# Optimization experiments

Hardware: AMD Instinct MI355X
Metric: run time of the kernel (lower is better)

## Reference

```python
import jax, jax.numpy as jnp
import numpy as np

N = 100_000      # nodes
E = 1_600_000    # edges (avg degree 16)
IN = 128         # in_feats
HID = 256        # hidden_feats
OUT = 160        # final fc output
EPS = 1e-5       # BatchNorm1d eps


def setup_inputs() -> dict:
    key = jax.random.key(0)
    ks = jax.random.split(key, 11)
    s = 0.02
    return {
        "features": jax.random.normal(ks[0], (N, IN), jnp.float32),
        "src": jax.random.randint(ks[1], (E,), 0, N, dtype=jnp.int32),
        "dst": jax.random.randint(ks[2], (E,), 0, N, dtype=jnp.int32),
        "edge_w": jax.random.uniform(ks[3], (E,), jnp.float32),
        "W_self": jax.random.normal(ks[4], (IN, HID), jnp.float32) * s,
        "W_neigh": jax.random.normal(ks[5], (IN, HID), jnp.float32) * s,
        "bias": jnp.zeros((HID,), jnp.float32),
        "gamma": jnp.ones((HID,), jnp.float32),
        "beta": jnp.zeros((HID,), jnp.float32),
        "fc_W": jax.random.normal(ks[6], (HID, OUT), jnp.float32) * s,
        "fc_b": jnp.zeros((OUT,), jnp.float32),
    }


def reference(features, src, dst, edge_w, W_self, W_neigh, bias, gamma, beta, fc_W, fc_b):
    # SAGEConv 'mean' with edge_weight: mean over incoming edges of src_feat * w
    msg = features[src] * edge_w[:, None]                       # [E, IN]
    ssum = jax.ops.segment_sum(msg, dst, num_segments=N)        # [N, IN]
    deg = jax.ops.segment_sum(jnp.ones((E,), features.dtype), dst, num_segments=N)
    neigh = ssum / jnp.maximum(deg, 1.0)[:, None]               # isolated nodes -> 0
    # rst = fc_self(h) + fc_neigh(neigh) + bias, then activation, then norm (DGL order)
    rst = features @ W_self + neigh @ W_neigh + bias            # [N, HID]
    rst = jax.nn.relu(rst)
    mu = rst.mean(axis=0)
    var = rst.var(axis=0)                                       # biased, as BatchNorm1d training
    rst = (rst - mu) * jax.lax.rsqrt(var + EPS) * gamma + beta
    return rst @ fc_W + fc_b                                    # [N, OUT]
```

## Files before the change

### kernel.cpp

```cpp
#include <hip/hip_runtime.h>
#include <hip/hip_fp16.h>

#define N_NODES 100000
#define N_EDGES 1600000
#define IN_F    128
#define HID_F   256
#define OUT_F   160
#define BN_EPS  1e-5f

#define EPB     4096
#define NCHUNK  ((N_EDGES + EPB - 1) / EPB)
#define NBKT    256
#define NPP2    391
#define BCAP2   8192
#define NSUB    (N_NODES / 32)
#define G1_GRID 512
#define NT2     ((N_NODES + 63) / 64)
#define G2_GRID 512
#define CVT_BLOCKS ((N_NODES * IN_F / 8 + 255) / 256)

typedef __attribute__((ext_vector_type(8))) short bf16x8;
typedef __attribute__((ext_vector_type(4))) float f32x4;
typedef __attribute__((ext_vector_type(2))) float f32x2;

static __device__ inline unsigned short f2bf(float x) {
  unsigned u = __float_as_uint(x);
  return (unsigned short)((u + 0x7fffu + ((u >> 16) & 1u)) >> 16);
}
static __device__ inline unsigned f2bf_pair(float lo, float hi) {
  return (unsigned)f2bf(lo) | ((unsigned)f2bf(hi) << 16);
}
static __device__ inline float bf_lo(unsigned u) {
  return __uint_as_float(u << 16);
}
static __device__ inline float bf_hi(unsigned u) {
  return __uint_as_float(u & 0xffff0000u);
}

#if __has_builtin(__builtin_amdgcn_cvt_f32_fp8)
#define FP8_DEC(d, s) __builtin_amdgcn_cvt_f32_fp8((int)(d), (s))
#else
static __device__ inline float FP8_DEC(unsigned d, int s) {
  unsigned b = (d >> (s * 8)) & 0xffu;
  unsigned em = b & 0x7fu;
  float mag = (em >= 8) ? __uint_as_float((em << 20) + (120u << 23))
                        : (float)em * 0.001953125f;
  return (b & 0x80u) ? -mag : mag;
}
#endif

#if __has_builtin(__builtin_amdgcn_cvt_pk_f32_fp8)
template <bool HI>
static __device__ inline f32x2 FP8_DEC2(unsigned d) {
  return __builtin_amdgcn_cvt_pk_f32_fp8((int)d, HI);
}
#else
template <bool HI>
static __device__ inline f32x2 FP8_DEC2(unsigned d) {
  f32x2 r;
  r.x = FP8_DEC(d, HI ? 2 : 0);
  r.y = FP8_DEC(d, HI ? 3 : 1);
  return r;
}
#endif

static __device__ inline void PK_FMA(f32x2& acc, f32x2 a, f32x2 b) {
#if defined(__gfx950__) || defined(__gfx942__) || defined(__gfx90a__) || \
    defined(__gfx940__) || defined(__gfx941__)
  asm("v_pk_fma_f32 %0, %1, %2, %0" : "+v"(acc) : "v"(a), "v"(b));
#else
  acc.x = fmaf(a.x, b.x, acc.x);
  acc.y = fmaf(a.y, b.y, acc.y);
#endif
}

#if __has_builtin(__builtin_amdgcn_cvt_pk_fp8_f32)
static __device__ inline unsigned fp8_pack4(float a, float b, float c, float d) {
  int p = __builtin_amdgcn_cvt_pk_fp8_f32(a, b, 0, false);
  p = __builtin_amdgcn_cvt_pk_fp8_f32(c, d, p, true);
  return (unsigned)p;
}
#else
static __device__ inline unsigned fp8_enc1(float x) {
  unsigned u = __float_as_uint(x);
  unsigned s = (u >> 24) & 0x80u;
  float ax = fabsf(x);
  if (ax >= 448.f) return s | 0x7eu;
  if (ax < 0.015625f) {
    unsigned m = (unsigned)(ax * 512.f + 0.5f);
    return s | (m > 7u ? 7u : m);
  }
  unsigned b = __float_as_uint(ax);
  b += 0x7ffffu + ((b >> 20) & 1u);
  unsigned exp = (b >> 23) - 120u;
  unsigned man = (b >> 20) & 7u;
  return s | (exp << 3) | man;
}
static __device__ inline unsigned fp8_pack4(float a, float b, float c, float d) {
  return fp8_enc1(a) | (fp8_enc1(b) << 8) | (fp8_enc1(c) << 16) |
         (fp8_enc1(d) << 24);
}
#endif

__global__ __launch_bounds__(256) void k_bucket(
    const int* __restrict__ src, const int* __restrict__ dst,
    const float* __restrict__ ew, int* __restrict__ gcnt,
    uint2* __restrict__ bucket) {
  __shared__ int bcnt[NBKT];
  __shared__ int bcur[NBKT];
  const int tid = threadIdx.x;
  const int e0 = blockIdx.x * EPB;
  bcnt[tid] = 0;
  __syncthreads();
  int ed[16];
  unsigned pd[16];
#pragma unroll
  for (int i = 0; i < 16; ++i) {
    int e = e0 + i * 256 + tid;
    int d = -1;
    unsigned p = 0;
    if (e < N_EDGES) {
      d = dst[e];
      unsigned hb = (unsigned)__half_as_ushort(__float2half(ew[e])) & 0x7fffu;
      p = ((unsigned)src[e] << 15) | hb;
      atomicAdd(&bcnt[d / NPP2], 1);
    }
    ed[i] = d;
    pd[i] = p;
  }
  __syncthreads();
  bcur[tid] = atomicAdd(&gcnt[tid], bcnt[tid]);
  __syncthreads();
#pragma unroll
  for (int i = 0; i < 16; ++i) {
    if (ed[i] >= 0) {
      int b = ed[i] / NPP2;
      int pos = atomicAdd(&bcur[b], 1);
      if (pos < BCAP2)
        bucket[(size_t)b * BCAP2 + pos] = make_uint2((unsigned)ed[i], pd[i]);
    }
  }
}

__global__ __launch_bounds__(256) void k_csr(
    const uint2* __restrict__ bucket, const int* __restrict__ gcnt,
    int* __restrict__ offs, unsigned* __restrict__ pairs) {
  __shared__ int cnt[512];
  __shared__ int wred[4];
  const int b = blockIdx.x;
  const int tid = threadIdx.x;
  const int lo = b * NPP2;
  const int n = min(gcnt[b], BCAP2);
  const uint2* bp = bucket + (size_t)b * BCAP2;

  int v = (tid < b) ? gcnt[tid] : 0;
  int x = v;
#pragma unroll
  for (int off = 1; off < 64; off <<= 1) x += __shfl_xor(x, off, 64);
  if ((tid & 63) == 0) wred[tid >> 6] = x;
  cnt[tid] = 0;
  cnt[tid + 256] = 0;
  __syncthreads();
  const int base = wred[0] + wred[1] + wred[2] + wred[3];

  for (int i = tid; i < n; i += 256)
    atomicAdd(&cnt[(int)bp[i].x - lo], 1);
  __syncthreads();

  if (tid < 64) {
    int carry = 0;
#pragma unroll
    for (int c = 0; c < 8; ++c) {
      int cv = cnt[c * 64 + tid];
      int cx = cv;
#pragma unroll
      for (int off = 1; off < 64; off <<= 1) {
        int q = __shfl_up(cx, off, 64);
        if (tid >= off) cx += q;
      }
      cnt[c * 64 + tid] = carry + cx - cv;
      carry += __shfl(cx, 63, 64);
    }
  }
  __syncthreads();

  for (int j = tid; j < NPP2; j += 256) {
    int node = lo + j;
    if (node < N_NODES) offs[node] = base + cnt[j];
  }
  if (b == 0 && tid == 0) offs[N_NODES] = N_EDGES;
  __syncthreads();

  for (int i = tid; i < n; i += 256) {
    uint2 it = bp[i];
    int r = atomicAdd(&cnt[(int)it.x - lo], 1);
    pairs[base + r] = it.y;
  }
}

__global__ __launch_bounds__(256) void k_convert(
    const float* __restrict__ feat, unsigned* __restrict__ A1u,
    unsigned* __restrict__ Af8u, const float* __restrict__ Wself,
    const float* __restrict__ Wneigh, unsigned short* __restrict__ W1T) {
  if (blockIdx.x >= CVT_BLOCKS) {
    int c = blockIdx.x - CVT_BLOCKS;
    int k = threadIdx.x;
    float v = (k < 128) ? Wself[(size_t)k * HID_F + c]
                        : Wneigh[(size_t)(k - 128) * HID_F + c];
    W1T[(size_t)c * 256 + k] = f2bf(v);
    return;
  }
  long long idx = (long long)blockIdx.x * 256 + threadIdx.x;
  long long fidx = idx * 8;
  if (fidx >= (long long)N_NODES * IN_F) return;
  int node = (int)(fidx >> 7);
  int c0 = (int)(fidx & 127);
  float4 f0 = *reinterpret_cast<const float4*>(feat + fidx);
  float4 f1 = *reinterpret_cast<const float4*>(feat + fidx + 4);
  uint4 o;
  o.x = f2bf_pair(f0.x, f0.y);
  o.y = f2bf_pair(f0.z, f0.w);
  o.z = f2bf_pair(f1.x, f1.y);
  o.w = f2bf_pair(f1.z, f1.w);
  *reinterpret_cast<uint4*>(A1u + (size_t)node * 128 + (c0 >> 1)) = o;
  uint2 q;
  q.x = fp8_pack4(f0.x, f0.y, f0.z, f0.w);
  q.y = fp8_pack4(f1.x, f1.y, f1.z, f1.w);
  *reinterpret_cast<uint2*>(Af8u + (size_t)node * 32 + (c0 >> 2)) = q;
}

__global__ __launch_bounds__(256) void k_gather(
    const int* __restrict__ offs, const unsigned* __restrict__ pairs,
    const unsigned* __restrict__ Af8u, unsigned* __restrict__ A1u) {
  int node = blockIdx.x * 4 + (threadIdx.x >> 6);
  if (node >= N_NODES) return;
  const int lane = threadIdx.x & 63;
  const int g = lane >> 4;
  const int cl = lane & 15;
  const int start = offs[node], end = offs[node + 1];
  const int deg = end - start;
  const unsigned* fbase = Af8u + cl * 2;

  f32x2 acc2[4];
#pragma unroll
  for (int i = 0; i < 4; ++i) acc2[i] = (f32x2){0.f, 0.f};

  for (int k0 = start; k0 < end; k0 += 64) {
    unsigned pr = 0;
    if (k0 + lane < end) pr = pairs[k0 + lane];
    const int cnt = min(64, end - k0);
    const int nsteps = (cnt + 3) >> 2;
    for (int t = 0; t < nsteps; t += 2) {
      unsigned uu0 = (unsigned)__shfl((int)pr, 4 * t + g, 64);
      unsigned uu1 = (unsigned)__shfl((int)pr, 4 * (t + 1) + g, 64);
      int s0 = (int)(uu0 >> 15);
      int s1 = (int)(uu1 >> 15);
      float w0 = __half2float(__ushort_as_half((unsigned short)(uu0 & 0x7fffu)));
      float w1 = __half2float(__ushort_as_half((unsigned short)(uu1 & 0x7fffu)));
      f32x2 wv0 = (f32x2){w0, w0};
      f32x2 wv1 = (f32x2){w1, w1};
      uint2 f0 = *reinterpret_cast<const uint2*>(fbase + (size_t)s0 * 32);
      uint2 f1 = *reinterpret_cast<const uint2*>(fbase + (size_t)s1 * 32);
      PK_FMA(acc2[0], wv0, FP8_DEC2<false>(f0.x));
      PK_FMA(acc2[1], wv0, FP8_DEC2<true>(f0.x));
      PK_FMA(acc2[2], wv0, FP8_DEC2<false>(f0.y));
      PK_FMA(acc2[3], wv0, FP8_DEC2<true>(f0.y));
      PK_FMA(acc2[0], wv1, FP8_DEC2<false>(f1.x));
      PK_FMA(acc2[1], wv1, FP8_DEC2<true>(f1.x));
      PK_FMA(acc2[2], wv1, FP8_DEC2<false>(f1.y));
      PK_FMA(acc2[3], wv1, FP8_DEC2<true>(f1.y));
    }
  }

#pragma unroll
  for (int i = 0; i < 4; ++i) {
    acc2[i].x += __shfl_xor(acc2[i].x, 16, 64);
    acc2[i].x += __shfl_xor(acc2[i].x, 32, 64);
    acc2[i].y += __shfl_xor(acc2[i].y, 16, 64);
    acc2[i].y += __shfl_xor(acc2[i].y, 32, 64);
  }

  if (g == 0) {
    const float inv = (deg > 0) ? (1.0f / (float)deg) : 0.f;
    uint4 o;
    o.x = f2bf_pair(acc2[0].x * inv, acc2[0].y * inv);
    o.y = f2bf_pair(acc2[1].x * inv, acc2[1].y * inv);
    o.z = f2bf_pair(acc2[2].x * inv, acc2[2].y * inv);
    o.w = f2bf_pair(acc2[3].x * inv, acc2[3].y * inv);
    *reinterpret_cast<uint4*>(A1u + (size_t)node * 128 + 64 + cl * 4) = o;
  }
}

__global__ __launch_bounds__(256, 2) void k_gemm1(
    const unsigned short* __restrict__ A1, const unsigned short* __restrict__ W1T,
    const float* __restrict__ bias, unsigned short* __restrict__ y,
    float* __restrict__ colpart) {
  __shared__ unsigned short sh[4 * 32 * 72];
  const int lane = threadIdx.x & 63;
  const int wid = threadIdx.x >> 6;
  const int l16 = lane & 15, lk = lane >> 4;
  const int h0 = wid * 64;
  unsigned short* shw = sh + wid * 32 * 72;

  bf16x8 wreg[8][4];
#pragma unroll
  for (int ks = 0; ks < 8; ++ks)
#pragma unroll
    for (int m = 0; m < 4; ++m)
      wreg[ks][m] = *reinterpret_cast<const bf16x8*>(
          W1T + (size_t)(h0 + m * 16 + l16) * 256 + ks * 32 + lk * 8);

  float4 bias4[4];
#pragma unroll
  for (int m = 0; m < 4; ++m)
    bias4[m] = *reinterpret_cast<const float4*>(bias + h0 + m * 16 + lk * 4);

  float sacc[4][4] = {};
  float qacc[4][4] = {};

  for (int t = blockIdx.x; t < NSUB; t += G1_GRID) {
    const int nbase = t * 32;
    const unsigned short* arow0 = A1 + (size_t)(nbase + l16) * 256 + lk * 8;
    const unsigned short* arow1 = A1 + (size_t)(nbase + 16 + l16) * 256 + lk * 8;

    f32x4 acc[4][2];
#pragma unroll
    for (int m = 0; m < 4; ++m)
#pragma unroll
      for (int n = 0; n < 2; ++n) acc[m][n] = (f32x4){0.f, 0.f, 0.f, 0.f};

#pragma unroll
    for (int ks = 0; ks < 8; ++ks) {
      bf16x8 a0 = *reinterpret_cast<const bf16x8*>(arow0 + ks * 32);
      bf16x8 a1 = *reinterpret_cast<const bf16x8*>(arow1 + ks * 32);
#pragma unroll
      for (int m = 0; m < 4; ++m) {
        acc[m][0] = __builtin_amdgcn_mfma_f32_16x16x32_bf16(
            wreg[ks][m], a0, acc[m][0], 0, 0, 0);
        acc[m][1] = __builtin_amdgcn_mfma_f32_16x16x32_bf16(
            wreg[ks][m], a1, acc[m][1], 0, 0, 0);
      }
    }

#pragma unroll
    for (int m = 0; m < 4; ++m) {
#pragma unroll
      for (int n = 0; n < 2; ++n) {
        float t0 = fmaxf(acc[m][n][0] + bias4[m].x, 0.f);
        float t1 = fmaxf(acc[m][n][1] + bias4[m].y, 0.f);
        float t2 = fmaxf(acc[m][n][2] + bias4[m].z, 0.f);
        float t3 = fmaxf(acc[m][n][3] + bias4[m].w, 0.f);
        uint2 pk;
        pk.x = f2bf_pair(t0, t1);
        pk.y = f2bf_pair(t2, t3);
        *reinterpret_cast<uint2*>(
            &shw[(n * 16 + l16) * 72 + m * 16 + lk * 4]) = pk;
        sacc[m][0] += t0; sacc[m][1] += t1; sacc[m][2] += t2; sacc[m][3] += t3;
        qacc[m][0] = fmaf(t0, t0, qacc[m][0]);
        qacc[m][1] = fmaf(t1, t1, qacc[m][1]);
        qacc[m][2] = fmaf(t2, t2, qacc[m][2]);
        qacc[m][3] = fmaf(t3, t3, qacc[m][3]);
      }
    }

#pragma unroll
    for (int j = 0; j < 4; ++j) {
      int row = j * 8 + (lane >> 3);
      int chunk = lane & 7;
      uint4 v = *reinterpret_cast<const uint4*>(&shw[row * 72 + chunk * 8]);
      *reinterpret_cast<uint4*>(
          y + (size_t)(nbase + row) * 256 + h0 + chunk * 8) = v;
    }
  }

#pragma unroll
  for (int m = 0; m < 4; ++m) {
#pragma unroll
    for (int r = 0; r < 4; ++r) {
      float s = sacc[m][r], q = qacc[m][r];
      s += __shfl_xor(s, 1, 64); s += __shfl_xor(s, 2, 64);
      s += __shfl_xor(s, 4, 64); s += __shfl_xor(s, 8, 64);
      q += __shfl_xor(q, 1, 64); q += __shfl_xor(q, 2, 64);
      q += __shfl_xor(q, 4, 64); q += __shfl_xor(q, 8, 64);
      if (l16 == 0) {
        int h = h0 + m * 16 + lk * 4 + r;
        colpart[(size_t)blockIdx.x * 512 + h] = s;
        colpart[(size_t)blockIdx.x * 512 + 256 + h] = q;
      }
    }
  }
}

__global__ __launch_bounds__(256) void k_redstats(
    const float* __restrict__ colpart, float* __restrict__ colsum,
    float* __restrict__ colsq) {
  const int h = threadIdx.x;
  float s = 0.f, q = 0.f;
  for (int j = blockIdx.x; j < G1_GRID; j += gridDim.x) {
    s += colpart[(size_t)j * 512 + h];
    q += colpart[(size_t)j * 512 + 256 + h];
  }
  atomicAdd(&colsum[h], s);
  atomicAdd(&colsq[h], q);
}

__global__ __launch_bounds__(256) void k_finalize(
    const float* __restrict__ colsum, const float* __restrict__ colsq,
    const float* __restrict__ gamma, const float* __restrict__ beta,
    const float* __restrict__ fcW, const float* __restrict__ fcb,
    unsigned short* __restrict__ W2T, float* __restrict__ b2) {
  const float invN = 1.0f / (float)N_NODES;
  if (blockIdx.x < 192) {
    int o = blockIdx.x, h = threadIdx.x;
    unsigned short v = 0;
    if (o < OUT_F) {
      float mu = colsum[h] * invN;
      float var = colsq[h] * invN - mu * mu;
      float rs = rsqrtf(var + BN_EPS) * gamma[h];
      v = f2bf(fcW[(size_t)h * OUT_F + o] * rs);
    }
    W2T[(size_t)o * 256 + h] = v;
  } else if (threadIdx.x < OUT_F) {
    int o = threadIdx.x;
    float acc = fcb[o];
    for (int h = 0; h < HID_F; ++h) {
      float mu = colsum[h] * invN;
      float var = colsq[h] * invN - mu * mu;
      float rs = rsqrtf(var + BN_EPS) * gamma[h];
      acc += (beta[h] - mu * rs) * fcW[(size_t)h * OUT_F + o];
    }
    b2[o] = acc;
  }
}

__global__ __launch_bounds__(256, 2) void k_gemm2(
    const unsigned short* __restrict__ y, const unsigned short* __restrict__ W2T,
    const float* __restrict__ b2, float* __restrict__ out) {
  const int lane = threadIdx.x & 63;
  const int wid = threadIdx.x >> 6;
  const int l16 = lane & 15, lk = lane >> 4;
  const int wn = wid & 1;
  const int o0 = (wid >> 1) * 80;

  bf16x8 wreg[8][5];
#pragma unroll
  for (int ks = 0; ks < 8; ++ks)
#pragma unroll
    for (int m = 0; m < 5; ++m)
      wreg[ks][m] = *reinterpret_cast<const bf16x8*>(
          W2T + (size_t)(o0 + m * 16 + l16) * 256 + ks * 32 + lk * 8);

  float4 b24[5];
#pragma unroll
  for (int m = 0; m < 5; ++m)
    b24[m] = *reinterpret_cast<const float4*>(b2 + o0 + m * 16 + lk * 4);

  for (int t = blockIdx.x; t < NT2; t += G2_GRID) {
    const int nb = t * 64 + wn * 32;
    const int r0 = min(nb + l16, N_NODES - 1);
    const int r1 = min(nb + 16 + l16, N_NODES - 1);

    f32x4 acc[5][2];
#pragma unroll
    for (int m = 0; m < 5; ++m)
#pragma unroll
      for (int n = 0; n < 2; ++n) acc[m][n] = (f32x4){0.f, 0.f, 0.f, 0.f};

#pragma unroll
    for (int ks = 0; ks < 8; ++ks) {
      bf16x8 bf0 = *reinterpret_cast<const bf16x8*>(
          y + (size_t)r0 * 256 + ks * 32 + lk * 8);
      bf16x8 bf1 = *reinterpret_cast<const bf16x8*>(
          y + (size_t)r1 * 256 + ks * 32 + lk * 8);
#pragma unroll
      for (int m = 0; m < 5; ++m) {
        acc[m][0] = __builtin_amdgcn_mfma_f32_16x16x32_bf16(
            wreg[ks][m], bf0, acc[m][0], 0, 0, 0);
        acc[m][1] = __builtin_amdgcn_mfma_f32_16x16x32_bf16(
            wreg[ks][m], bf1, acc[m][1], 0, 0, 0);
      }
    }

#pragma unroll
    for (int n = 0; n < 2; ++n) {
      const int fb = nb + n * 16;
      if (fb < N_NODES) {
#pragma unroll
        for (int m = 0; m < 5; ++m) {
          float4 v;
          v.x = acc[m][n][0] + b24[m].x;
          v.y = acc[m][n][1] + b24[m].y;
          v.z = acc[m][n][2] + b24[m].z;
          v.w = acc[m][n][3] + b24[m].w;
          *reinterpret_cast<float4*>(
              out + (size_t)(fb + l16) * OUT_F + o0 + m * 16 + lk * 4) = v;
        }
      }
    }
  }
}

extern "C" void kernel_launch(void* const* d_in, const int* in_sizes, int n_in,
                              void* d_out, int out_size, void* d_ws,
                              size_t ws_size, hipStream_t stream) {
  const float* feat   = (const float*)d_in[0];
  const int*   src    = (const int*)d_in[1];
  const int*   dst    = (const int*)d_in[2];
  const float* ew     = (const float*)d_in[3];
  const float* Wself  = (const float*)d_in[4];
  const float* Wneigh = (const float*)d_in[5];
  const float* bias   = (const float*)d_in[6];
  const float* gamma  = (const float*)d_in[7];
  const float* beta   = (const float*)d_in[8];
  const float* fcW    = (const float*)d_in[9];
  const float* fcb    = (const float*)d_in[10];
  float* out = (float*)d_out;

  char* ws = (char*)d_ws;
  int*            gcnt    = (int*)(ws + 0);
  float*          colsum  = (float*)(ws + 1024);
  float*          colsq   = (float*)(ws + 2048);
  int*            offs    = (int*)(ws + 4224);
  unsigned*       pairs   = (unsigned*)(ws + 404480);
  uint2*          bucket  = (uint2*)(ws + 6804480);
  unsigned*       Af8u    = (unsigned*)(ws + 23581696);
  unsigned*       A1u     = (unsigned*)(ws + 36381696);
  unsigned short* A1      = (unsigned short*)(ws + 36381696);
  unsigned short* W1T     = (unsigned short*)(ws + 87581696);
  unsigned short* W2T     = (unsigned short*)(ws + 87712768);
  float*          b2      = (float*)(ws + 87811072);
  unsigned short* y       = (unsigned short*)(ws + 87811712);
  float*          colpart = (float*)(ws + 139011712);

  hipMemsetAsync(ws, 0, 3072, stream);

  dim3 b256(256);
  k_convert<<<dim3(CVT_BLOCKS + 256), b256, 0, stream>>>(
      feat, A1u, Af8u, Wself, Wneigh, W1T);
  k_bucket<<<dim3(NCHUNK), b256, 0, stream>>>(src, dst, ew, gcnt, bucket);
  k_csr<<<dim3(NBKT), b256, 0, stream>>>(bucket, gcnt, offs, pairs);
  k_gather<<<dim3((N_NODES + 3) / 4), b256, 0, stream>>>(
      offs, pairs, Af8u, A1u);
  k_gemm1<<<dim3(G1_GRID), b256, 0, stream>>>(A1, W1T, bias, y, colpart);
  k_redstats<<<dim3(32), b256, 0, stream>>>(colpart, colsum, colsq);
  k_finalize<<<dim3(193), b256, 0, stream>>>(
      colsum, colsq, gamma, beta, fcW, fcb, W2T, b2);
  k_gemm2<<<dim3(G2_GRID), b256, 0, stream>>>(y, W2T, b2, out);
}
```

Before: 210.0 us.

## Replace persistent GEMM grids with one tile per block and streamed weights

Both GEMM kernels drop their grid-stride persistent loop and the register-resident weight cache. Each block now handles exactly one 32- or 64-node tile and loads weight fragments from global memory inside the k-loop. The intent is to cut register pressure and raise occupancy and launch parallelism. In exchange, every block re-reads the full weight slice through the caches, and per-block column partials grow to one entry per tile, so the stats reduction reads much more data and colpart needs a larger workspace.

```diff
diff --git a/kernel.cpp b/kernel.cpp
--- a/kernel.cpp
+++ b/kernel.cpp
@@ -14,9 +14,7 @@
 #define NPP2    391
 #define BCAP2   8192
 #define NSUB    (N_NODES / 32)
-#define G1_GRID 512
 #define NT2     ((N_NODES + 63) / 64)
-#define G2_GRID 512
 #define CVT_BLOCKS ((N_NODES * IN_F / 8 + 255) / 256)
 
 typedef __attribute__((ext_vector_type(8))) short bf16x8;
@@ -29,12 +27,6 @@
 }
 static __device__ inline unsigned f2bf_pair(float lo, float hi) {
   return (unsigned)f2bf(lo) | ((unsigned)f2bf(hi) << 16);
-}
-static __device__ inline float bf_lo(unsigned u) {
-  return __uint_as_float(u << 16);
-}
-static __device__ inline float bf_hi(unsigned u) {
-  return __uint_as_float(u & 0xffff0000u);
 }
 
 #if __has_builtin(__builtin_amdgcn_cvt_f32_fp8)
@@ -302,75 +294,61 @@
   const int h0 = wid * 64;
   unsigned short* shw = sh + wid * 32 * 72;
 
-  bf16x8 wreg[8][4];
-#pragma unroll
-  for (int ks = 0; ks < 8; ++ks)
-#pragma unroll
-    for (int m = 0; m < 4; ++m)
-      wreg[ks][m] = *reinterpret_cast<const bf16x8*>(
+  const int nbase = blockIdx.x * 32;
+  const unsigned short* arow0 = A1 + (size_t)(nbase + l16) * 256 + lk * 8;
+  const unsigned short* arow1 = A1 + (size_t)(nbase + 16 + l16) * 256 + lk * 8;
+
+  f32x4 acc[4][2];
+#pragma unroll
+  for (int m = 0; m < 4; ++m)
+#pragma unroll
+    for (int n = 0; n < 2; ++n) acc[m][n] = (f32x4){0.f, 0.f, 0.f, 0.f};
+
+#pragma unroll
+  for (int ks = 0; ks < 8; ++ks) {
+    bf16x8 a0 = *reinterpret_cast<const bf16x8*>(arow0 + ks * 32);
+    bf16x8 a1 = *reinterpret_cast<const bf16x8*>(arow1 + ks * 32);
+#pragma unroll
+    for (int m = 0; m < 4; ++m) {
+      bf16x8 w = *reinterpret_cast<const bf16x8*>(
           W1T + (size_t)(h0 + m * 16 + l16) * 256 + ks * 32 + lk * 8);
-
-  float4 bias4[4];
-#pragma unroll
-  for (int m = 0; m < 4; ++m)
-    bias4[m] = *reinterpret_cast<const float4*>(bias + h0 + m * 16 + lk * 4);
+      acc[m][0] = __builtin_amdgcn_mfma_f32_16x16x32_bf16(w, a0, acc[m][0], 0, 0, 0);
+      acc[m][1] = __builtin_amdgcn_mfma_f32_16x16x32_bf16(w, a1, acc[m][1], 0, 0, 0);
+    }
+  }
 
   float sacc[4][4] = {};
   float qacc[4][4] = {};
 
-  for (int t = blockIdx.x; t < NSUB; t += G1_GRID) {
-    const int nbase = t * 32;
-    const unsigned short* arow0 = A1 + (size_t)(nbase + l16) * 256 + lk * 8;
-    const unsigned short* arow1 = A1 + (size_t)(nbase + 16 + l16) * 256 + lk * 8;
-
-    f32x4 acc[4][2];
-#pragma unroll
-    for (int m = 0; m < 4; ++m)
-#pragma unroll
-      for (int n = 0; n < 2; ++n) acc[m][n] = (f32x4){0.f, 0.f, 0.f, 0.f};
-
-#pragma unroll
-    for (int ks = 0; ks < 8; ++ks) {
-      bf16x8 a0 = *reinterpret_cast<const bf16x8*>(arow0 + ks * 32);
-      bf16x8 a1 = *reinterpret_cast<const bf16x8*>(arow1 + ks * 32);
-#pragma unroll
-      for (int m = 0; m < 4; ++m) {
-        acc[m][0] = __builtin_amdgcn_mfma_f32_16x16x32_bf16(
-            wreg[ks][m], a0, acc[m][0], 0, 0, 0);
-        acc[m][1] = __builtin_amdgcn_mfma_f32_16x16x32_bf16(
-            wreg[ks][m], a1, acc[m][1], 0, 0, 0);
-      }
-    }
-
-#pragma unroll
-    for (int m = 0; m < 4; ++m) {
-#pragma unroll
-      for (int n = 0; n < 2; ++n) {
-        float t0 = fmaxf(acc[m][n][0] + bias4[m].x, 0.f);
-        float t1 = fmaxf(acc[m][n][1] + bias4[m].y, 0.f);
-        float t2 = fmaxf(acc[m][n][2] + bias4[m].z, 0.f);
-        float t3 = fmaxf(acc[m][n][3] + bias4[m].w, 0.f);
-        uint2 pk;
-        pk.x = f2bf_pair(t0, t1);
-        pk.y = f2bf_pair(t2, t3);
-        *reinterpret_cast<uint2*>(
-            &shw[(n * 16 + l16) * 72 + m * 16 + lk * 4]) = pk;
-        sacc[m][0] += t0; sacc[m][1] += t1; sacc[m][2] += t2; sacc[m][3] += t3;
-        qacc[m][0] = fmaf(t0, t0, qacc[m][0]);
-        qacc[m][1] = fmaf(t1, t1, qacc[m][1]);
-        qacc[m][2] = fmaf(t2, t2, qacc[m][2]);
-        qacc[m][3] = fmaf(t3, t3, qacc[m][3]);
-      }
-    }
-
-#pragma unroll
-    for (int j = 0; j < 4; ++j) {
-      int row = j * 8 + (lane >> 3);
-      int chunk = lane & 7;
-      uint4 v = *reinterpret_cast<const uint4*>(&shw[row * 72 + chunk * 8]);
-      *reinterpret_cast<uint4*>(
-          y + (size_t)(nbase + row) * 256 + h0 + chunk * 8) = v;
-    }
+#pragma unroll
+  for (int m = 0; m < 4; ++m) {
+    const float4 b4 = *reinterpret_cast<const float4*>(bias + h0 + m * 16 + lk * 4);
+#pragma unroll
+    for (int n = 0; n < 2; ++n) {
+      float t0 = fmaxf(acc[m][n][0] + b4.x, 0.f);
+      float t1 = fmaxf(acc[m][n][1] + b4.y, 0.f);
+      float t2 = fmaxf(acc[m][n][2] + b4.z, 0.f);
+      float t3 = fmaxf(acc[m][n][3] + b4.w, 0.f);
+      uint2 pk;
+      pk.x = f2bf_pair(t0, t1);
+      pk.y = f2bf_pair(t2, t3);
+      *reinterpret_cast<uint2*>(
+          &shw[(n * 16 + l16) * 72 + m * 16 + lk * 4]) = pk;
+      sacc[m][0] += t0; sacc[m][1] += t1; sacc[m][2] += t2; sacc[m][3] += t3;
+      qacc[m][0] = fmaf(t0, t0, qacc[m][0]);
+      qacc[m][1] = fmaf(t1, t1, qacc[m][1]);
+      qacc[m][2] = fmaf(t2, t2, qacc[m][2]);
+      qacc[m][3] = fmaf(t3, t3, qacc[m][3]);
+    }
+  }
+
+#pragma unroll
+  for (int j = 0; j < 4; ++j) {
+    int row = j * 8 + (lane >> 3);
+    int chunk = lane & 7;
+    uint4 v = *reinterpret_cast<const uint4*>(&shw[row * 72 + chunk * 8]);
+    *reinterpret_cast<uint4*>(
+        y + (size_t)(nbase + row) * 256 + h0 + chunk * 8) = v;
   }
 
 #pragma unroll
@@ -396,7 +374,7 @@
     float* __restrict__ colsq) {
   const int h = threadIdx.x;
   float s = 0.f, q = 0.f;
-  for (int j = blockIdx.x; j < G1_GRID; j += gridDim.x) {
+  for (int j = blockIdx.x; j < NSUB; j += gridDim.x) {
     s += colpart[(size_t)j * 512 + h];
     q += colpart[(size_t)j * 512 + 256 + h];
   }
@@ -442,59 +420,45 @@
   const int wn = wid & 1;
   const int o0 = (wid >> 1) * 80;
 
-  bf16x8 wreg[8][5];
-#pragma unroll
-  for (int ks = 0; ks < 8; ++ks)
-#pragma unroll
-    for (int m = 0; m < 5; ++m)
-      wreg[ks][m] = *reinterpret_cast<const bf16x8*>(
+  const int nb = blockIdx.x * 64 + wn * 32;
+  const int r0 = min(nb + l16, N_NODES - 1);
+  const int r1 = min(nb + 16 + l16, N_NODES - 1);
+  const unsigned short* yrow0 = y + (size_t)r0 * 256 + lk * 8;
+  const unsigned short* yrow1 = y + (size_t)r1 * 256 + lk * 8;
+
+  f32x4 acc[5][2];
+#pragma unroll
+  for (int m = 0; m < 5; ++m)
+#pragma unroll
+    for (int n = 0; n < 2; ++n) acc[m][n] = (f32x4){0.f, 0.f, 0.f, 0.f};
+
+#pragma unroll
+  for (int ks = 0; ks < 8; ++ks) {
+    bf16x8 a0 = *reinterpret_cast<const bf16x8*>(yrow0 + ks * 32);
+    bf16x8 a1 = *reinterpret_cast<const bf16x8*>(yrow1 + ks * 32);
+#pragma unroll
+    for (int m = 0; m < 5; ++m) {
+      bf16x8 w = *reinterpret_cast<const bf16x8*>(
           W2T + (size_t)(o0 + m * 16 + l16) * 256 + ks * 32 + lk * 8);
-
-  float4 b24[5];
-#pragma unroll
-  for (int m = 0; m < 5; ++m)
-    b24[m] = *reinterpret_cast<const float4*>(b2 + o0 + m * 16 + lk * 4);
-
-  for (int t = blockIdx.x; t < NT2; t += G2_GRID) {
-    const int nb = t * 64 + wn * 32;
-    const int r0 = min(nb + l16, N_NODES - 1);
-    const int r1 = min(nb + 16 + l16, N_NODES - 1);
-
-    f32x4 acc[5][2];
-#pragma unroll
-    for (int m = 0; m < 5; ++m)
-#pragma unroll
-      for (int n = 0; n < 2; ++n) acc[m][n] = (f32x4){0.f, 0.f, 0.f, 0.f};
-
-#pragma unroll
-    for (int ks = 0; ks < 8; ++ks) {
-      bf16x8 bf0 = *reinterpret_cast<const bf16x8*>(
-          y + (size_t)r0 * 256 + ks * 32 + lk * 8);
-      bf16x8 bf1 = *reinterpret_cast<const bf16x8*>(
-          y + (size_t)r1 * 256 + ks * 32 + lk * 8);
+      acc[m][0] = __builtin_amdgcn_mfma_f32_16x16x32_bf16(w, a0, acc[m][0], 0, 0, 0);
+      acc[m][1] = __builtin_amdgcn_mfma_f32_16x16x32_bf16(w, a1, acc[m][1], 0, 0, 0);
+    }
+  }
+
+#pragma unroll
+  for (int n = 0; n < 2; ++n) {
+    const int fb = nb + n * 16;
+    if (fb < N_NODES) {
 #pragma unroll
       for (int m = 0; m < 5; ++m) {
-        acc[m][0] = __builtin_amdgcn_mfma_f32_16x16x32_bf16(
-            wreg[ks][m], bf0, acc[m][0], 0, 0, 0);
-        acc[m][1] = __builtin_amdgcn_mfma_f32_16x16x32_bf16(
-            wreg[ks][m], bf1, acc[m][1], 0, 0, 0);
-      }
-    }
-
-#pragma unroll
-    for (int n = 0; n < 2; ++n) {
-      const int fb = nb + n * 16;
-      if (fb < N_NODES) {
-#pragma unroll
-        for (int m = 0; m < 5; ++m) {
-          float4 v;
-          v.x = acc[m][n][0] + b24[m].x;
-          v.y = acc[m][n][1] + b24[m].y;
-          v.z = acc[m][n][2] + b24[m].z;
-          v.w = acc[m][n][3] + b24[m].w;
-          *reinterpret_cast<float4*>(
-              out + (size_t)(fb + l16) * OUT_F + o0 + m * 16 + lk * 4) = v;
-        }
+        const float4 b4 = *reinterpret_cast<const float4*>(b2 + o0 + m * 16 + lk * 4);
+        float4 v;
+        v.x = acc[m][n][0] + b4.x;
+        v.y = acc[m][n][1] + b4.y;
+        v.z = acc[m][n][2] + b4.z;
+        v.w = acc[m][n][3] + b4.w;
+        *reinterpret_cast<float4*>(
+            out + (size_t)(fb + l16) * OUT_F + o0 + m * 16 + lk * 4) = v;
       }
     }
   }
@@ -541,9 +505,9 @@
   k_csr<<<dim3(NBKT), b256, 0, stream>>>(bucket, gcnt, offs, pairs);
   k_gather<<<dim3((N_NODES + 3) / 4), b256, 0, stream>>>(
       offs, pairs, Af8u, A1u);
-  k_gemm1<<<dim3(G1_GRID), b256, 0, stream>>>(A1, W1T, bias, y, colpart);
-  k_redstats<<<dim3(32), b256, 0, stream>>>(colpart, colsum, colsq);
+  k_gemm1<<<dim3(NSUB), b256, 0, stream>>>(A1, W1T, bias, y, colpart);
+  k_redstats<<<dim3(64), b256, 0, stream>>>(colpart, colsum, colsq);
   k_finalize<<<dim3(193), b256, 0, stream>>>(
       colsum, colsq, gamma, beta, fcW, fcb, W2T, b2);
-  k_gemm2<<<dim3(G2_GRID), b256, 0, stream>>>(y, W2T, b2, out);
-}
+  k_gemm2<<<dim3(NT2), b256, 0, stream>>>(y, W2T, b2, out);
+}
```

After: 274.5 us. +30.7%, slower.
